# Kernel tuning notes

Measured on AMD Instinct MI355X. Metric: run time of the kernel, lower is better.

Reference implementation:

```python
import jax, jax.numpy as jnp
import numpy as np

N_NODES = 50000
N_EDGES = 800000
N_GRAPHS = 128
HEADS = 4
HDIM = 32
N_CLASSES = 10
LEAKY_ALPHA = 0.2


def setup_inputs() -> dict:
    key = jax.random.key(0)
    ks = jax.random.split(key, 12)
    src = jax.random.randint(ks[0], (N_EDGES,), 0, N_NODES, dtype=jnp.int32)
    # guarantee every node has in-degree >= 1 so 3/deg is finite
    dst_tail = jax.random.randint(ks[1], (N_EDGES - N_NODES,), 0, N_NODES, dtype=jnp.int32)
    dst = jnp.concatenate([jnp.arange(N_NODES, dtype=jnp.int32), dst_tail])
    graph_ids = jnp.sort(jax.random.randint(ks[2], (N_NODES,), 0, N_GRAPHS, dtype=jnp.int32))
    s = 0.1
    return {
        "src": src,
        "dst": dst,
        "graph_ids": graph_ids,
        "W1": jax.random.normal(ks[3], (4, HEADS * HDIM), jnp.float32) * s,
        "al1": jax.random.normal(ks[4], (HEADS, HDIM), jnp.float32) * s,
        "ar1": jax.random.normal(ks[5], (HEADS, HDIM), jnp.float32) * s,
        "W2": jax.random.normal(ks[6], (HEADS * HDIM, HEADS * HDIM), jnp.float32) * s,
        "al2": jax.random.normal(ks[7], (HEADS, HDIM), jnp.float32) * s,
        "ar2": jax.random.normal(ks[8], (HEADS, HDIM), jnp.float32) * s,
        "Wc": jax.random.normal(ks[9], (HEADS * HDIM, N_CLASSES), jnp.float32) * s,
        "bc": jax.random.normal(ks[10], (N_CLASSES,), jnp.float32) * s,
    }


def _gat_layer(x, src, dst, W, al, ar):
    # x: [N, Fin]; W: [Fin, H*D]; al, ar: [H, D]
    n = x.shape[0]
    ft = (x @ W).reshape(n, HEADS, HDIM)                       # [N, H, D]
    a1 = jnp.einsum("nhd,hd->nh", ft, al)                      # [N, H]
    a2 = jnp.einsum("nhd,hd->nh", ft, ar)                      # [N, H]
    e = jax.nn.leaky_relu(a1[src] + a2[dst], LEAKY_ALPHA)      # [E, H]
    # segment softmax over incoming edges of each dst node
    m = jax.ops.segment_max(e, dst, num_segments=n)            # [N, H]
    m = jax.lax.stop_gradient(m)
    ex = jnp.exp(e - m[dst])                                   # [E, H]
    denom = jax.ops.segment_sum(ex, dst, num_segments=n)       # [N, H]
    alpha = ex / denom[dst]                                    # [E, H]
    # gather-multiply-scatter aggregation
    out = jax.ops.segment_sum(ft[src] * alpha[:, :, None], dst, num_segments=n)  # [N, H, D]
    return jax.nn.relu(out.reshape(n, HEADS * HDIM))


def reference(src, dst, graph_ids, W1, al1, ar1, W2, al2, ar2, Wc, bc):
    n = N_NODES
    ones_e = jnp.ones(src.shape[0], jnp.float32)
    deg = jax.ops.segment_sum(ones_e, dst, num_segments=n)     # in-degrees [N]
    h = jnp.stack(
        [deg, (deg - 3.0 > 0).astype(jnp.float32), 3.0 / deg, (deg - 4.0 > 0).astype(jnp.float32)],
        axis=1,
    )                                                          # [N, 4]
    h = _gat_layer(h, src, dst, W1, al1, ar1)                  # [N, H*D]
    h = _gat_layer(h, src, dst, W2, al2, ar2)                  # [N, H*D]
    # mean_nodes: per-graph mean pooling
    gsum = jax.ops.segment_sum(h, graph_ids, num_segments=N_GRAPHS)
    cnt = jax.ops.segment_sum(jnp.ones(n, jnp.float32), graph_ids, num_segments=N_GRAPHS)
    gmean = gsum / jnp.maximum(cnt, 1.0)[:, None]              # [G, H*D]
    return jax.nn.sigmoid(gmean @ Wc + bc)                     # [G, n_classes]
```

## Files before the change

kernel.cpp:

```cpp
#include <hip/hip_runtime.h>
#include <hip/hip_fp16.h>
#include <math.h>

#define HEADS 4
#define HDIM 32
#define FDIM 128
#define NGRAPH 128
#define NCLASS 10

#define NBW 128
#define NBP 512
#define SLICE 4096

typedef _Float16 h4_t __attribute__((ext_vector_type(4)));
typedef float f4_t __attribute__((ext_vector_type(4)));
typedef float f2_t __attribute__((ext_vector_type(2)));

__device__ __forceinline__ float lrelu(float x) { return fmaxf(x, 0.2f * x); }

__global__ void k_wfrag(const float* __restrict__ W2, __half* __restrict__ Wfrag,
                        float* __restrict__ gsum, int* __restrict__ gcnt,
                        int* __restrict__ bcnt) {
    int gid = blockIdx.x * 256 + threadIdx.x;
    ((float4*)gsum)[gid] = make_float4(0.f, 0.f, 0.f, 0.f);
    if (gid < NGRAPH) gcnt[gid] = 0;
    if (gid < NBP) bcnt[gid] = 0;
    int fid = gid >> 6, l = gid & 63;
    int ks = fid >> 3, t = fid & 7;
    int k0 = ks * 16 + 4 * (l >> 4);
    int n0 = t * 16 + (l & 15);
    __half2 lo = __floats2half2_rn(W2[(k0 + 0) * FDIM + n0], W2[(k0 + 1) * FDIM + n0]);
    __half2 hi = __floats2half2_rn(W2[(k0 + 2) * FDIM + n0], W2[(k0 + 3) * FDIM + n0]);
    size_t base = ((size_t)fid * 64 + l) * 4;
    *(__half2*)(Wfrag + base)     = lo;
    *(__half2*)(Wfrag + base + 2) = hi;
}

__global__ void k_bhist(const int* __restrict__ dst, int E, int* __restrict__ bcnt) {
    __shared__ int lcnt[NBP];
    int tid = threadIdx.x;
    for (int i = tid; i < NBP; i += 256) lcnt[i] = 0;
    __syncthreads();
    int beg = blockIdx.x * SLICE, end = min(E, beg + SLICE);
    for (int i = beg + tid; i < end; i += 256)
        atomicAdd(&lcnt[dst[i] >> 7], 1);
    __syncthreads();
    for (int i = tid; i < NBP; i += 256)
        if (lcnt[i]) atomicAdd(&bcnt[i], lcnt[i]);
}

__global__ void k_bscan2(const int* __restrict__ bcnt, int* __restrict__ bbase,
                         int* __restrict__ bcur) {
    __shared__ int ws[4];
    int tid = threadIdx.x, lane = tid & 63, w = tid >> 6;
    int c0 = bcnt[2 * tid], c1 = bcnt[2 * tid + 1];
    int t = c0 + c1;
    int incl = t;
    #pragma unroll
    for (int off = 1; off < 64; off <<= 1) {
        int y = __shfl_up(incl, off);
        if (lane >= off) incl += y;
    }
    if (lane == 63) ws[w] = incl;
    __syncthreads();
    int wpre = 0;
    #pragma unroll
    for (int j = 0; j < 4; ++j) if (j < w) wpre += ws[j];
    int ex = wpre + (incl - t);
    bbase[2 * tid] = ex;          bcur[2 * tid] = ex;
    bbase[2 * tid + 1] = ex + c0; bcur[2 * tid + 1] = ex + c0;
}

__global__ __launch_bounds__(256) void k_part(const int* __restrict__ src,
        const int* __restrict__ dst, int E, int* __restrict__ bcur,
        int2* __restrict__ part) {
    __shared__ int lcnt[NBP];
    __shared__ int loff[NBP];
    __shared__ int lpos[NBP];
    __shared__ int2 staged[SLICE];
    __shared__ int tgt[SLICE];
    __shared__ int ws[4];
    int tid = threadIdx.x, lane = tid & 63, w = tid >> 6;
    int beg = blockIdx.x * SLICE, end = min(E, beg + SLICE);
    int m = end - beg;
    for (int i = tid; i < NBP; i += 256) lcnt[i] = 0;
    __syncthreads();
    for (int i = beg + tid; i < end; i += 256)
        atomicAdd(&lcnt[dst[i] >> 7], 1);
    __syncthreads();
    int c0 = lcnt[2 * tid], c1 = lcnt[2 * tid + 1];
    int t = c0 + c1;
    int incl = t;
    #pragma unroll
    for (int off = 1; off < 64; off <<= 1) {
        int y = __shfl_up(incl, off);
        if (lane >= off) incl += y;
    }
    if (lane == 63) ws[w] = incl;
    __syncthreads();
    int wpre = 0;
    #pragma unroll
    for (int j = 0; j < 4; ++j) if (j < w) wpre += ws[j];
    int ex = wpre + (incl - t);
    loff[2 * tid] = ex; loff[2 * tid + 1] = ex + c0;
    if (c0) lpos[2 * tid] = atomicAdd(&bcur[2 * tid], c0);
    if (c1) lpos[2 * tid + 1] = atomicAdd(&bcur[2 * tid + 1], c1);
    lcnt[2 * tid] = 0; lcnt[2 * tid + 1] = 0;
    __syncthreads();
    for (int i = beg + tid; i < end; i += 256) {
        int s = src[i], d = dst[i];
        int b = d >> 7;
        int idx = atomicAdd(&lcnt[b], 1);
        int slot = loff[b] + idx;
        staged[slot] = make_int2(s, d);
        tgt[slot] = lpos[b] + idx;
    }
    __syncthreads();
    for (int i = tid; i < m; i += 256)
        part[tgt[i]] = staged[i];
}

__global__ __launch_bounds__(256) void k_build(const int2* __restrict__ part,
        const int* __restrict__ bbase, const int* __restrict__ bcnt,
        const float* __restrict__ W1, const float* __restrict__ al,
        const float* __restrict__ ar, int* __restrict__ offs, int* __restrict__ csr,
        float* __restrict__ h4t, float* __restrict__ a1, float* __restrict__ a2,
        int n, int E) {
    __shared__ int ldeg[NBW];
    __shared__ int loffs[NBW];
    __shared__ int wtot[2];
    __shared__ float wla[16], wlr[16];
    int b = blockIdx.x, tid = threadIdx.x;
    int lane = tid & 63, w = tid >> 6;
    if (tid < NBW) ldeg[tid] = 0;
    if (tid < 32) {
        int k = (tid & 15) >> 2, h = tid & 3;
        const float* av = (tid < 16) ? al : ar;
        float s = 0.f;
        #pragma unroll
        for (int d = 0; d < 32; ++d) s += W1[k * FDIM + h * HDIM + d] * av[h * HDIM + d];
        if (tid < 16) wla[k * 4 + h] = s; else wlr[k * 4 + h] = s;
    }
    __syncthreads();
    int beg = bbase[b], end = beg + bcnt[b];
    for (int i = beg + tid; i < end; i += 256)
        atomicAdd(&ldeg[part[i].y & (NBW - 1)], 1);
    __syncthreads();
    int x = (tid < NBW) ? ldeg[tid] : 0;
    int incl = x;
    #pragma unroll
    for (int off = 1; off < 64; off <<= 1) {
        int y = __shfl_up(incl, off);
        if (lane >= off) incl += y;
    }
    if (tid < NBW && lane == 63) wtot[w] = incl;
    __syncthreads();
    if (tid < NBW) {
        int pre = incl - x;
        if (w == 1) pre += wtot[0];
        loffs[tid] = beg + pre;
        int v = b * NBW + tid;
        if (v < n) {
            offs[v] = beg + pre;
            float d = (float)x;
            float4 hv = make_float4(d, (d - 3.0f > 0.0f) ? 1.0f : 0.0f, 3.0f / d,
                                    (d - 4.0f > 0.0f) ? 1.0f : 0.0f);
            *(float4*)(h4t + v * 4) = hv;
            float4 o1, o2;
            #pragma unroll
            for (int h = 0; h < 4; ++h) {
                float s1 = hv.x * wla[0 + h] + hv.y * wla[4 + h] + hv.z * wla[8 + h] + hv.w * wla[12 + h];
                float s2 = hv.x * wlr[0 + h] + hv.y * wlr[4 + h] + hv.z * wlr[8 + h] + hv.w * wlr[12 + h];
                if (h == 0) { o1.x = s1; o2.x = s2; } else if (h == 1) { o1.y = s1; o2.y = s2; }
                else if (h == 2) { o1.z = s1; o2.z = s2; } else { o1.w = s1; o2.w = s2; }
            }
            *(float4*)(a1 + v * 4) = o1;
            *(float4*)(a2 + v * 4) = o2;
        }
    }
    if (b == 0 && tid == 0) offs[n] = E;
    __syncthreads();
    if (tid < NBW) ldeg[tid] = 0;
    __syncthreads();
    for (int i = beg + tid; i < end; i += 256) {
        int2 e = part[i];
        int lv = e.y & (NBW - 1);
        int p = atomicAdd(&ldeg[lv], 1);
        csr[loffs[lv] + p] = e.x;
    }
}

__global__ __launch_bounds__(256) void k_l2f(const int* __restrict__ offs,
        const int* __restrict__ csr, const float* __restrict__ h4t,
        const float* __restrict__ a1, const float* __restrict__ a2,
        const float* __restrict__ W1, const __half* __restrict__ Wfrag,
        const float* __restrict__ al, const float* __restrict__ ar,
        unsigned char* __restrict__ ft8, float* __restrict__ a1b,
        float* __restrict__ a2b, int n) {
    __shared__ __half Blds[64 * 64 * 4];
    __shared__ __half Alds[4][16 * 132];
    __shared__ float Slds[4][256];
    int tid = threadIdx.x, l = tid & 63, w = tid >> 6;
    int c = l & 15, g = l >> 4;

    #pragma unroll
    for (int i = 0; i < 8; ++i)
        ((float4*)Blds)[i * 256 + tid] = ((const float4*)Wfrag)[i * 256 + tid];

    int v0 = (blockIdx.x * 4 + w) * 16;

    for (int r4 = 0; r4 < 4; ++r4) {
        int v = v0 + r4 * 4 + g;
        bool vok = v < n;
        int beg = 0, end = 0;
        if (vok) { beg = offs[v]; end = offs[v + 1]; }
        int dg = end - beg;
        float4 a2v = vok ? *(const float4*)(a2 + v * 4) : make_float4(0, 0, 0, 0);
        float P[4][4], D[4];
        #pragma unroll
        for (int h = 0; h < 4; ++h) { D[h] = 0.f;
            #pragma unroll
            for (int d = 0; d < 4; ++d) P[h][d] = 0.f; }
        for (int base2 = 0; base2 < dg; base2 += 16) {
            if (base2 + c < dg) {
                int u = csr[beg + base2 + c];
                float4 a1u = *(const float4*)(a1 + u * 4);
                float4 f4  = *(const float4*)(h4t + u * 4);
                float wgt[4];
                wgt[0] = __expf(lrelu(a1u.x + a2v.x));
                wgt[1] = __expf(lrelu(a1u.y + a2v.y));
                wgt[2] = __expf(lrelu(a1u.z + a2v.z));
                wgt[3] = __expf(lrelu(a1u.w + a2v.w));
                #pragma unroll
                for (int h = 0; h < 4; ++h) {
                    D[h] += wgt[h];
                    P[h][0] = fmaf(wgt[h], f4.x, P[h][0]);
                    P[h][1] = fmaf(wgt[h], f4.y, P[h][1]);
                    P[h][2] = fmaf(wgt[h], f4.z, P[h][2]);
                    P[h][3] = fmaf(wgt[h], f4.w, P[h][3]);
                }
            }
        }
        #pragma unroll
        for (int off = 1; off < 16; off <<= 1) {
            #pragma unroll
            for (int h = 0; h < 4; ++h) {
                D[h] += __shfl_xor(D[h], off);
                #pragma unroll
                for (int d = 0; d < 4; ++d) P[h][d] += __shfl_xor(P[h][d], off);
            }
        }
        if (vok && c == 0) {
            #pragma unroll
            for (int h = 0; h < 4; ++h) {
                float r = 1.0f / D[h];
                #pragma unroll
                for (int d = 0; d < 4; ++d)
                    Slds[w][(r4 * 4 + g) * 16 + h * 4 + d] = P[h][d] * r;
            }
        }
    }

    float2 w1c[4];
    #pragma unroll
    for (int d = 0; d < 4; ++d) w1c[d] = *(const float2*)(W1 + d * FDIM + 2 * l);
    for (int jj = 0; jj < 16; ++jj) {
        float4 s = *(const float4*)(&Slds[w][jj * 16 + g * 4]);
        float t0 = s.x * w1c[0].x + s.y * w1c[1].x + s.z * w1c[2].x + s.w * w1c[3].x;
        float t1 = s.x * w1c[0].y + s.y * w1c[1].y + s.z * w1c[2].y + s.w * w1c[3].y;
        *(__half2*)(&Alds[w][jj * 132 + 2 * l]) = __floats2half2_rn(fmaxf(t0, 0.f), fmaxf(t1, 0.f));
    }
    __syncthreads();

    f4_t acc[8];
    #pragma unroll
    for (int t = 0; t < 8; ++t) acc[t] = (f4_t){0.f, 0.f, 0.f, 0.f};
    #pragma unroll
    for (int ks = 0; ks < 8; ++ks) {
        h4_t af = *(const h4_t*)(&Alds[w][c * 132 + ks * 16 + 4 * g]);
        #pragma unroll
        for (int t = 0; t < 8; ++t) {
            h4_t bf = *(const h4_t*)(&Blds[((ks * 8 + t) * 64 + l) * 4]);
            acc[t] = __builtin_amdgcn_mfma_f32_16x16x16f16(af, bf, acc[t], 0, 0, 0);
        }
    }

    #pragma unroll
    for (int t = 0; t < 8; ++t) {
        #pragma unroll
        for (int r = 0; r < 4; ++r) {
            int v = v0 + 4 * g + r;
            if (v < n) {
                int pk = __builtin_amdgcn_cvt_pk_fp8_f32(acc[t][r], acc[t][r], 0, false);
                ft8[(size_t)v * FDIM + t * 16 + c] = (unsigned char)(pk & 0xff);
            }
        }
    }
    float al0[4], al1v[4], ar0[4], ar1v[4];
    #pragma unroll
    for (int h = 0; h < 4; ++h) {
        al0[h] = al[h * 32 + c]; al1v[h] = al[h * 32 + 16 + c];
        ar0[h] = ar[h * 32 + c]; ar1v[h] = ar[h * 32 + 16 + c];
    }
    #pragma unroll
    for (int r = 0; r < 4; ++r) {
        int v = v0 + 4 * g + r;
        #pragma unroll
        for (int h = 0; h < 4; ++h) {
            float p1 = acc[2 * h][r] * al0[h] + acc[2 * h + 1][r] * al1v[h];
            float p2 = acc[2 * h][r] * ar0[h] + acc[2 * h + 1][r] * ar1v[h];
            #pragma unroll
            for (int off = 1; off < 16; off <<= 1) {
                p1 += __shfl_xor(p1, off);
                p2 += __shfl_xor(p2, off);
            }
            if (c == h && v < n) {
                a1b[v * 4 + h] = p1;
                a2b[v * 4 + h] = p2;
            }
        }
    }
}

__global__ void k_agg2(const int* __restrict__ offs, const int* __restrict__ csr,
                       const unsigned char* __restrict__ ft8, const float* __restrict__ a1,
                       const float* __restrict__ a2, __half* __restrict__ out, int n) {
    __shared__ float wlds[4][64 * 4];
    int tid = threadIdx.x, lane = tid & 63, w = tid >> 6;
    int v = blockIdx.x * 4 + w;
    if (v >= n) return;
    int beg = offs[v], end = offs[v + 1];
    int deg = end - beg;
    float4 a2v = *(const float4*)(a2 + v * 4);
    int h = lane >> 4;
    int f = 2 * lane;
    float2 acc = make_float2(0.f, 0.f);
    float4 dsum = make_float4(0.f, 0.f, 0.f, 0.f);
    float* wbuf = wlds[w];
    for (int base = 0; base < deg; base += 64) {
        int m = min(64, deg - base);
        int u = 0;
        float4 wgt = make_float4(0.f, 0.f, 0.f, 0.f);
        if (lane < m) {
            u = csr[beg + base + lane];
            float4 a1u = *(const float4*)(a1 + u * 4);
            wgt.x = __expf(lrelu(a1u.x + a2v.x));
            wgt.y = __expf(lrelu(a1u.y + a2v.y));
            wgt.z = __expf(lrelu(a1u.z + a2v.z));
            wgt.w = __expf(lrelu(a1u.w + a2v.w));
        }
        dsum.x += wgt.x; dsum.y += wgt.y; dsum.z += wgt.z; dsum.w += wgt.w;
        *(float4*)(wbuf + lane * 4) = wgt;
        int j = 0;
        for (; j + 4 <= m; j += 4) {
            int s0 = __builtin_amdgcn_readlane(u, j);
            int s1 = __builtin_amdgcn_readlane(u, j + 1);
            int s2 = __builtin_amdgcn_readlane(u, j + 2);
            int s3 = __builtin_amdgcn_readlane(u, j + 3);
            float w0 = wbuf[(j + 0) * 4 + h];
            float w1 = wbuf[(j + 1) * 4 + h];
            float w2 = wbuf[(j + 2) * 4 + h];
            float w3 = wbuf[(j + 3) * 4 + h];
            int b0 = *(const unsigned short*)(ft8 + (size_t)s0 * FDIM + f);
            int b1 = *(const unsigned short*)(ft8 + (size_t)s1 * FDIM + f);
            int b2 = *(const unsigned short*)(ft8 + (size_t)s2 * FDIM + f);
            int b3 = *(const unsigned short*)(ft8 + (size_t)s3 * FDIM + f);
            f2_t g0 = __builtin_amdgcn_cvt_pk_f32_fp8(b0, false);
            f2_t g1 = __builtin_amdgcn_cvt_pk_f32_fp8(b1, false);
            f2_t g2 = __builtin_amdgcn_cvt_pk_f32_fp8(b2, false);
            f2_t g3 = __builtin_amdgcn_cvt_pk_f32_fp8(b3, false);
            acc.x = fmaf(w0, g0[0], acc.x); acc.y = fmaf(w0, g0[1], acc.y);
            acc.x = fmaf(w1, g1[0], acc.x); acc.y = fmaf(w1, g1[1], acc.y);
            acc.x = fmaf(w2, g2[0], acc.x); acc.y = fmaf(w2, g2[1], acc.y);
            acc.x = fmaf(w3, g3[0], acc.x); acc.y = fmaf(w3, g3[1], acc.y);
        }
        for (; j < m; ++j) {
            int s0 = __builtin_amdgcn_readlane(u, j);
            float w0 = wbuf[j * 4 + h];
            int b0 = *(const unsigned short*)(ft8 + (size_t)s0 * FDIM + f);
            f2_t g0 = __builtin_amdgcn_cvt_pk_f32_fp8(b0, false);
            acc.x = fmaf(w0, g0[0], acc.x); acc.y = fmaf(w0, g0[1], acc.y);
        }
    }
    #pragma unroll
    for (int off = 1; off < 64; off <<= 1) {
        dsum.x += __shfl_xor(dsum.x, off);
        dsum.y += __shfl_xor(dsum.y, off);
        dsum.z += __shfl_xor(dsum.z, off);
        dsum.w += __shfl_xor(dsum.w, off);
    }
    float dh = (h < 2) ? (h == 0 ? dsum.x : dsum.y) : (h == 2 ? dsum.z : dsum.w);
    float r = 1.0f / dh;
    *(__half2*)(out + (size_t)v * FDIM + f) =
        __floats2half2_rn(fmaxf(acc.x * r, 0.f), fmaxf(acc.y * r, 0.f));
}

__global__ void k_pool(const __half* __restrict__ hbuf, const int* __restrict__ gid,
                       float* __restrict__ gsum, int* __restrict__ gcnt, int n) {
    const int STRIP = 32;
    int wv = (blockIdx.x * blockDim.x + threadIdx.x) >> 6;
    int lane = threadIdx.x & 63;
    int beg = wv * STRIP;
    if (beg >= n) return;
    int end = min(beg + STRIP, n);
    int f = 2 * lane;
    float2 acc = make_float2(0.f, 0.f);
    int cur = gid[beg];
    int cnt = 0;
    for (int i = beg; i < end; ++i) {
        int g = gid[i];
        if (g != cur) {
            atomicAdd(&gsum[cur * FDIM + f], acc.x);
            atomicAdd(&gsum[cur * FDIM + f + 1], acc.y);
            if (lane == 0) atomicAdd(&gcnt[cur], cnt);
            acc = make_float2(0.f, 0.f); cnt = 0; cur = g;
        }
        float2 x = __half22float2(*(const __half2*)(hbuf + (size_t)i * FDIM + f));
        acc.x += x.x; acc.y += x.y; cnt++;
    }
    atomicAdd(&gsum[cur * FDIM + f], acc.x);
    atomicAdd(&gsum[cur * FDIM + f + 1], acc.y);
    if (lane == 0) atomicAdd(&gcnt[cur], cnt);
}

__global__ void k_classify(const float* __restrict__ gsum, const int* __restrict__ gcnt,
                           const float* __restrict__ Wc, const float* __restrict__ bc,
                           float* __restrict__ out) {
    int idx = blockIdx.x * blockDim.x + threadIdx.x;
    if (idx >= NGRAPH * NCLASS) return;
    int g = idx / NCLASS, c = idx % NCLASS;
    float rc = 1.0f / fmaxf((float)gcnt[g], 1.0f);
    float s = bc[c];
    for (int k = 0; k < FDIM; ++k)
        s += gsum[g * FDIM + k] * rc * Wc[k * NCLASS + c];
    out[idx] = 1.0f / (1.0f + __expf(-s));
}

extern "C" void kernel_launch(void* const* d_in, const int* in_sizes, int n_in,
                              void* d_out, int out_size, void* d_ws, size_t ws_size,
                              hipStream_t stream) {
    const int*   src = (const int*)d_in[0];
    const int*   dst = (const int*)d_in[1];
    const int*   gid = (const int*)d_in[2];
    const float* W1  = (const float*)d_in[3];
    const float* al1 = (const float*)d_in[4];
    const float* ar1 = (const float*)d_in[5];
    const float* W2  = (const float*)d_in[6];
    const float* al2 = (const float*)d_in[7];
    const float* ar2 = (const float*)d_in[8];
    const float* Wc  = (const float*)d_in[9];
    const float* bc  = (const float*)d_in[10];
    float* out = (float*)d_out;
    const int E = in_sizes[0];
    const int N = in_sizes[2];

    char* ws = (char*)d_ws;
    size_t off = 0;
    auto alloc = [&](size_t bytes) -> void* {
        void* p = ws + off;
        off = (off + bytes + 255) & ~(size_t)255;
        return p;
    };
    int*    offs   = (int*)alloc((size_t)(N + 1) * 4);
    int*    csr    = (int*)alloc((size_t)E * 4);
    int2*   part   = (int2*)alloc((size_t)E * 8);
    int*    bcnt   = (int*)alloc(NBP * 4);
    int*    bbase  = (int*)alloc(NBP * 4);
    int*    bcur   = (int*)alloc(NBP * 4);
    float*  h4t    = (float*)alloc((size_t)N * 4 * 4);
    float*  a1     = (float*)alloc((size_t)N * HEADS * 4);
    float*  a2     = (float*)alloc((size_t)N * HEADS * 4);
    float*  a1b    = (float*)alloc((size_t)N * HEADS * 4);
    float*  a2b    = (float*)alloc((size_t)N * HEADS * 4);
    unsigned char* ft8 = (unsigned char*)alloc((size_t)N * FDIM);
    __half* hbuf   = (__half*)alloc((size_t)N * FDIM * 2);
    __half* Wfrag  = (__half*)alloc((size_t)FDIM * FDIM * 2);
    float*  gsum   = (float*)alloc((size_t)NGRAPH * FDIM * 4);
    int*    gcnt   = (int*)alloc((size_t)NGRAPH * 4);

    int pb_edges = (E + SLICE - 1) / SLICE;
    int nb2 = (N + NBW - 1) / NBW;

    k_wfrag<<<16, 256, 0, stream>>>(W2, Wfrag, gsum, gcnt, bcnt);
    k_bhist<<<pb_edges, 256, 0, stream>>>(dst, E, bcnt);
    k_bscan2<<<1, 256, 0, stream>>>(bcnt, bbase, bcur);
    k_part<<<pb_edges, 256, 0, stream>>>(src, dst, E, bcur, part);
    k_build<<<nb2, 256, 0, stream>>>(part, bbase, bcnt, W1, al1, ar1,
                                     offs, csr, h4t, a1, a2, N, E);
    k_l2f<<<(N + 63) / 64, 256, 0, stream>>>(offs, csr, h4t, a1, a2, W1, Wfrag,
                                             al2, ar2, ft8, a1b, a2b, N);
    k_agg2<<<(N + 3) / 4, 256, 0, stream>>>(offs, csr, ft8, a1b, a2b, hbuf, N);

    int pb = (((N + 31) / 32) + 3) / 4;
    k_pool<<<pb, 256, 0, stream>>>(hbuf, gid, gsum, gcnt, N);
    k_classify<<<(NGRAPH * NCLASS + 255) / 256, 256, 0, stream>>>(gsum, gcnt, Wc, bc, out);
}
```

Measured before the change: 140.7 us.

## Aggregate layer-2 GAT with 16-lane groups per node and 8-byte fp8 gathers

Restructures the second-layer aggregation so each 16-lane quarter-wavefront handles one destination node, with each lane gathering 8 fp8 features per edge as a single uint2 load instead of 2 bytes per lane across a full wavefront. Edge weights are now computed per lane for its own head, which removes the LDS weight buffer, the readlane broadcasts and the wave-wide denominator reduction. This targets wasted lanes at low in-degree (about 16 edges per node) and raises bytes per memory instruction. In exchange the exp and a1 loads are duplicated across the 4 lanes sharing a head, and edges are walked serially two at a time, so load imbalance between nodes in one wave can cause divergence.

```diff
diff --git a/kernel.cpp b/kernel.cpp
--- a/kernel.cpp
+++ b/kernel.cpp
@@ -322,77 +322,57 @@
     }
 }
 
-__global__ void k_agg2(const int* __restrict__ offs, const int* __restrict__ csr,
-                       const unsigned char* __restrict__ ft8, const float* __restrict__ a1,
-                       const float* __restrict__ a2, __half* __restrict__ out, int n) {
-    __shared__ float wlds[4][64 * 4];
+__global__ __launch_bounds__(256) void k_agg2(const int* __restrict__ offs,
+        const int* __restrict__ csr, const unsigned char* __restrict__ ft8,
+        const float* __restrict__ a1, const float* __restrict__ a2,
+        __half* __restrict__ out, int n) {
     int tid = threadIdx.x, lane = tid & 63, w = tid >> 6;
-    int v = blockIdx.x * 4 + w;
+    int qw = lane >> 4, ql = lane & 15;
+    int v = blockIdx.x * 16 + w * 4 + qw;
     if (v >= n) return;
     int beg = offs[v], end = offs[v + 1];
-    int deg = end - beg;
-    float4 a2v = *(const float4*)(a2 + v * 4);
-    int h = lane >> 4;
-    int f = 2 * lane;
-    float2 acc = make_float2(0.f, 0.f);
-    float4 dsum = make_float4(0.f, 0.f, 0.f, 0.f);
-    float* wbuf = wlds[w];
-    for (int base = 0; base < deg; base += 64) {
-        int m = min(64, deg - base);
-        int u = 0;
-        float4 wgt = make_float4(0.f, 0.f, 0.f, 0.f);
-        if (lane < m) {
-            u = csr[beg + base + lane];
-            float4 a1u = *(const float4*)(a1 + u * 4);
-            wgt.x = __expf(lrelu(a1u.x + a2v.x));
-            wgt.y = __expf(lrelu(a1u.y + a2v.y));
-            wgt.z = __expf(lrelu(a1u.z + a2v.z));
-            wgt.w = __expf(lrelu(a1u.w + a2v.w));
-        }
-        dsum.x += wgt.x; dsum.y += wgt.y; dsum.z += wgt.z; dsum.w += wgt.w;
-        *(float4*)(wbuf + lane * 4) = wgt;
-        int j = 0;
-        for (; j + 4 <= m; j += 4) {
-            int s0 = __builtin_amdgcn_readlane(u, j);
-            int s1 = __builtin_amdgcn_readlane(u, j + 1);
-            int s2 = __builtin_amdgcn_readlane(u, j + 2);
-            int s3 = __builtin_amdgcn_readlane(u, j + 3);
-            float w0 = wbuf[(j + 0) * 4 + h];
-            float w1 = wbuf[(j + 1) * 4 + h];
-            float w2 = wbuf[(j + 2) * 4 + h];
-            float w3 = wbuf[(j + 3) * 4 + h];
-            int b0 = *(const unsigned short*)(ft8 + (size_t)s0 * FDIM + f);
-            int b1 = *(const unsigned short*)(ft8 + (size_t)s1 * FDIM + f);
-            int b2 = *(const unsigned short*)(ft8 + (size_t)s2 * FDIM + f);
-            int b3 = *(const unsigned short*)(ft8 + (size_t)s3 * FDIM + f);
-            f2_t g0 = __builtin_amdgcn_cvt_pk_f32_fp8(b0, false);
-            f2_t g1 = __builtin_amdgcn_cvt_pk_f32_fp8(b1, false);
-            f2_t g2 = __builtin_amdgcn_cvt_pk_f32_fp8(b2, false);
-            f2_t g3 = __builtin_amdgcn_cvt_pk_f32_fp8(b3, false);
-            acc.x = fmaf(w0, g0[0], acc.x); acc.y = fmaf(w0, g0[1], acc.y);
-            acc.x = fmaf(w1, g1[0], acc.x); acc.y = fmaf(w1, g1[1], acc.y);
-            acc.x = fmaf(w2, g2[0], acc.x); acc.y = fmaf(w2, g2[1], acc.y);
-            acc.x = fmaf(w3, g3[0], acc.x); acc.y = fmaf(w3, g3[1], acc.y);
-        }
-        for (; j < m; ++j) {
-            int s0 = __builtin_amdgcn_readlane(u, j);
-            float w0 = wbuf[j * 4 + h];
-            int b0 = *(const unsigned short*)(ft8 + (size_t)s0 * FDIM + f);
-            f2_t g0 = __builtin_amdgcn_cvt_pk_f32_fp8(b0, false);
-            acc.x = fmaf(w0, g0[0], acc.x); acc.y = fmaf(w0, g0[1], acc.y);
-        }
-    }
-    #pragma unroll
-    for (int off = 1; off < 64; off <<= 1) {
-        dsum.x += __shfl_xor(dsum.x, off);
-        dsum.y += __shfl_xor(dsum.y, off);
-        dsum.z += __shfl_xor(dsum.z, off);
-        dsum.w += __shfl_xor(dsum.w, off);
-    }
-    float dh = (h < 2) ? (h == 0 ? dsum.x : dsum.y) : (h == 2 ? dsum.z : dsum.w);
-    float r = 1.0f / dh;
-    *(__half2*)(out + (size_t)v * FDIM + f) =
-        __floats2half2_rn(fmaxf(acc.x * r, 0.f), fmaxf(acc.y * r, 0.f));
+    int h = ql >> 2;
+    float a2h = a2[v * 4 + h];
+    float acc[8];
+    #pragma unroll
+    for (int k = 0; k < 8; ++k) acc[k] = 0.f;
+    float dsum = 0.f;
+    const unsigned char* fbase = ft8 + (size_t)ql * 8;
+    int j = beg;
+    for (; j + 2 <= end; j += 2) {
+        int s0 = csr[j], s1 = csr[j + 1];
+        float w0 = __expf(lrelu(a1[s0 * 4 + h] + a2h));
+        float w1 = __expf(lrelu(a1[s1 * 4 + h] + a2h));
+        uint2 b0 = *(const uint2*)(fbase + (size_t)s0 * FDIM);
+        uint2 b1 = *(const uint2*)(fbase + (size_t)s1 * FDIM);
+        dsum += w0 + w1;
+        f2_t g;
+        g = __builtin_amdgcn_cvt_pk_f32_fp8(b0.x, false); acc[0] = fmaf(w0, g[0], acc[0]); acc[1] = fmaf(w0, g[1], acc[1]);
+        g = __builtin_amdgcn_cvt_pk_f32_fp8(b0.x, true);  acc[2] = fmaf(w0, g[0], acc[2]); acc[3] = fmaf(w0, g[1], acc[3]);
+        g = __builtin_amdgcn_cvt_pk_f32_fp8(b0.y, false); acc[4] = fmaf(w0, g[0], acc[4]); acc[5] = fmaf(w0, g[1], acc[5]);
+        g = __builtin_amdgcn_cvt_pk_f32_fp8(b0.y, true);  acc[6] = fmaf(w0, g[0], acc[6]); acc[7] = fmaf(w0, g[1], acc[7]);
+        g = __builtin_amdgcn_cvt_pk_f32_fp8(b1.x, false); acc[0] = fmaf(w1, g[0], acc[0]); acc[1] = fmaf(w1, g[1], acc[1]);
+        g = __builtin_amdgcn_cvt_pk_f32_fp8(b1.x, true);  acc[2] = fmaf(w1, g[0], acc[2]); acc[3] = fmaf(w1, g[1], acc[3]);
+        g = __builtin_amdgcn_cvt_pk_f32_fp8(b1.y, false); acc[4] = fmaf(w1, g[0], acc[4]); acc[5] = fmaf(w1, g[1], acc[5]);
+        g = __builtin_amdgcn_cvt_pk_f32_fp8(b1.y, true);  acc[6] = fmaf(w1, g[0], acc[6]); acc[7] = fmaf(w1, g[1], acc[7]);
+    }
+    for (; j < end; ++j) {
+        int s0 = csr[j];
+        float w0 = __expf(lrelu(a1[s0 * 4 + h] + a2h));
+        uint2 b0 = *(const uint2*)(fbase + (size_t)s0 * FDIM);
+        dsum += w0;
+        f2_t g;
+        g = __builtin_amdgcn_cvt_pk_f32_fp8(b0.x, false); acc[0] = fmaf(w0, g[0], acc[0]); acc[1] = fmaf(w0, g[1], acc[1]);
+        g = __builtin_amdgcn_cvt_pk_f32_fp8(b0.x, true);  acc[2] = fmaf(w0, g[0], acc[2]); acc[3] = fmaf(w0, g[1], acc[3]);
+        g = __builtin_amdgcn_cvt_pk_f32_fp8(b0.y, false); acc[4] = fmaf(w0, g[0], acc[4]); acc[5] = fmaf(w0, g[1], acc[5]);
+        g = __builtin_amdgcn_cvt_pk_f32_fp8(b0.y, true);  acc[6] = fmaf(w0, g[0], acc[6]); acc[7] = fmaf(w0, g[1], acc[7]);
+    }
+    float r = 1.0f / dsum;
+    __half2 o[4];
+    #pragma unroll
+    for (int k = 0; k < 4; ++k)
+        o[k] = __floats2half2_rn(fmaxf(acc[2 * k] * r, 0.f), fmaxf(acc[2 * k + 1] * r, 0.f));
+    *(float4*)(out + (size_t)v * FDIM + ql * 8) = *(float4*)o;
 }
 
 __global__ void k_pool(const __half* __restrict__ hbuf, const int* __restrict__ gid,
@@ -489,7 +469,7 @@
                                      offs, csr, h4t, a1, a2, N, E);
     k_l2f<<<(N + 63) / 64, 256, 0, stream>>>(offs, csr, h4t, a1, a2, W1, Wfrag,
                                              al2, ar2, ft8, a1b, a2b, N);
-    k_agg2<<<(N + 3) / 4, 256, 0, stream>>>(offs, csr, ft8, a1b, a2b, hbuf, N);
+    k_agg2<<<(N + 15) / 16, 256, 0, stream>>>(offs, csr, ft8, a1b, a2b, hbuf, N);
 
     int pb = (((N + 31) / 32) + 3) / 4;
     k_pool<<<pb, 256, 0, stream>>>(hbuf, gid, gsum, gcnt, N);
```

After: 134.6 us. -4.4%, faster.
